# Kernel optimization log

Hardware: AMD Instinct MI355X
Metric: run time of the kernel (lower is better)

## Reference

```python
import jax, jax.numpy as jnp
import numpy as np


def setup_inputs() -> dict:
    key = jax.random.key(0)
    k1, k2, k3, k4 = jax.random.split(key, 4)
    in_f, out_f, rank, tokens = 4096, 4096, 256, 8192
    bound = 1.0 / np.sqrt(in_f)
    x = jax.random.normal(k1, (tokens, in_f), dtype=jnp.float32)
    U = jax.random.uniform(k2, (out_f, rank), dtype=jnp.float32, minval=-bound, maxval=bound)
    V = jax.random.uniform(k3, (rank, in_f), dtype=jnp.float32, minval=-bound, maxval=bound)
    bias = jax.random.uniform(k4, (out_f,), dtype=jnp.float32, minval=-bound, maxval=bound)
    return {"x": x, "U": U, "V": V, "bias": bias}


def reference(x, U, V, bias):
    # Faithful to original: materialize W = U @ V, then F.linear(x, W, bias) = x @ W.T + bias
    W = U @ V                      # [out, in]
    return x @ W.T + bias          # [tokens, out]
```

## Files before the change

kernel.cpp:

```cpp
#include <hip/hip_runtime.h>
#include <stdint.h>

#define TOKENS 8192
#define INF    4096
#define OUTF   4096
#define RANK   256

typedef __attribute__((ext_vector_type(8))) short bf16x8;
typedef __attribute__((ext_vector_type(4))) float f32x4;

__device__ __forceinline__ unsigned short f2bf(float f) {
    union { float f; unsigned int u; } v; v.f = f;
    unsigned int r = v.u + 0x7FFFu + ((v.u >> 16) & 1u);
    return (unsigned short)(r >> 16);
}

__device__ __forceinline__ void gl_lds16(const void* g, void* l) {
    __builtin_amdgcn_global_load_lds(
        (const __attribute__((address_space(1))) unsigned int*)g,
        (__attribute__((address_space(3))) unsigned int*)l, 16, 0, 0);
}

__global__ void cvt4(const float4* __restrict__ va, ushort4* __restrict__ oa, int na,
                     const float4* __restrict__ vb, ushort4* __restrict__ ob) {
    int i = blockIdx.x * blockDim.x + threadIdx.x;
    float4 v;
    if (i < na) v = va[i]; else v = vb[i - na];
    ushort4 o;
    o.x = f2bf(v.x); o.y = f2bf(v.y); o.z = f2bf(v.z); o.w = f2bf(v.w);
    if (i < na) oa[i] = o; else ob[i - na] = o;
}

#define G1_BM 32
#define G1_BK 128
#define A1_STR 136

__device__ __forceinline__ void g1_stageV(const unsigned short* __restrict__ Vb,
                                          unsigned short* vdst, int kk,
                                          int wid, int lane) {
    #pragma unroll
    for (int j = 0; j < 8; ++j) {
        int r0  = wid * 32 + j * 4;
        int row = r0 + (lane >> 4);
        int c   = (lane & 15) ^ (row & 7);
        gl_lds16(Vb + (size_t)row * INF + kk + c * 8, vdst + r0 * G1_BK);
    }
}

__device__ __forceinline__ void g1_pack(float4 a, float4 b, unsigned short* dst) {
    union { bf16x8 v; unsigned short s[8]; } pk;
    pk.s[0] = f2bf(a.x); pk.s[1] = f2bf(a.y);
    pk.s[2] = f2bf(a.z); pk.s[3] = f2bf(a.w);
    pk.s[4] = f2bf(b.x); pk.s[5] = f2bf(b.y);
    pk.s[6] = f2bf(b.z); pk.s[7] = f2bf(b.w);
    *(bf16x8*)dst = pk.v;
}

__device__ __forceinline__ void g1_compute(f32x4 (&acc)[2][2],
                                           const unsigned short* vbuf,
                                           const unsigned short* abuf,
                                           int l15, int quad, int wid) {
    const int rr0 = wid * 32 + l15;
    const int sw  = l15 & 7;
    #pragma unroll
    for (int ks = 0; ks < 4; ++ks) {
        int p = ((ks * 4 + quad) ^ sw) * 8;
        bf16x8 v0 = *(const bf16x8*)&vbuf[rr0 * G1_BK + p];
        bf16x8 v1 = *(const bf16x8*)&vbuf[(rr0 + 16) * G1_BK + p];
        bf16x8 b0 = *(const bf16x8*)&abuf[l15 * A1_STR + ks * 32 + quad * 8];
        bf16x8 b1 = *(const bf16x8*)&abuf[(16 + l15) * A1_STR + ks * 32 + quad * 8];
        acc[0][0] = __builtin_amdgcn_mfma_f32_16x16x32_bf16(v0, b0, acc[0][0], 0, 0, 0);
        acc[0][1] = __builtin_amdgcn_mfma_f32_16x16x32_bf16(v0, b1, acc[0][1], 0, 0, 0);
        acc[1][0] = __builtin_amdgcn_mfma_f32_16x16x32_bf16(v1, b0, acc[1][0], 0, 0, 0);
        acc[1][1] = __builtin_amdgcn_mfma_f32_16x16x32_bf16(v1, b1, acc[1][1], 0, 0, 0);
    }
}

__global__ __launch_bounds__(512) void gemm1(const float* __restrict__ x,
                                             const unsigned short* __restrict__ Vb,
                                             unsigned short* __restrict__ T) {
    __shared__ __align__(16) unsigned short V0[RANK * G1_BK];
    __shared__ __align__(16) unsigned short V1[RANK * G1_BK];
    __shared__ __align__(16) unsigned short A0[G1_BM * A1_STR];
    __shared__ __align__(16) unsigned short A1[G1_BM * A1_STR];

    const int tid  = threadIdx.x;
    const int lane = tid & 63;
    const int wid  = tid >> 6;
    const int m0   = blockIdx.x * G1_BM;
    const int l15  = lane & 15;
    const int quad = lane >> 4;

    const int arow = tid >> 4;
    const int aseg = tid & 15;
    const float* xp = x + (size_t)(m0 + arow) * INF + aseg * 8;
    unsigned short* aw0 = &A0[arow * A1_STR + aseg * 8];
    unsigned short* aw1 = &A1[arow * A1_STR + aseg * 8];

    f32x4 acc[2][2];
    #pragma unroll
    for (int i = 0; i < 2; ++i)
        #pragma unroll
        for (int j = 0; j < 2; ++j) acc[i][j] = (f32x4){0.f, 0.f, 0.f, 0.f};

    g1_stageV(Vb, V0, 0, wid, lane);
    float4 xr0 = *(const float4*)(xp);
    float4 xr1 = *(const float4*)(xp + 4);
    g1_pack(xr0, xr1, aw0);

    for (int t = 0; t < 30; t += 2) {
        __syncthreads();
        g1_stageV(Vb, V1, (t + 1) * G1_BK, wid, lane);
        xr0 = *(const float4*)(xp + (t + 1) * G1_BK);
        xr1 = *(const float4*)(xp + (t + 1) * G1_BK + 4);
        g1_compute(acc, V0, A0, l15, quad, wid);
        g1_pack(xr0, xr1, aw1);

        __syncthreads();
        g1_stageV(Vb, V0, (t + 2) * G1_BK, wid, lane);
        xr0 = *(const float4*)(xp + (t + 2) * G1_BK);
        xr1 = *(const float4*)(xp + (t + 2) * G1_BK + 4);
        g1_compute(acc, V1, A1, l15, quad, wid);
        g1_pack(xr0, xr1, aw0);
    }
    __syncthreads();
    g1_stageV(Vb, V1, 31 * G1_BK, wid, lane);
    xr0 = *(const float4*)(xp + 31 * G1_BK);
    xr1 = *(const float4*)(xp + 31 * G1_BK + 4);
    g1_compute(acc, V0, A0, l15, quad, wid);
    g1_pack(xr0, xr1, aw1);
    __syncthreads();
    g1_compute(acc, V1, A1, l15, quad, wid);

    #pragma unroll
    for (int mv = 0; mv < 2; ++mv) {
        #pragma unroll
        for (int mx = 0; mx < 2; ++mx) {
            int m = m0 + mx * 16 + l15;
            int n = wid * 32 + mv * 16 + quad * 4;
            ushort4 o;
            o.x = f2bf(acc[mv][mx][0]); o.y = f2bf(acc[mv][mx][1]);
            o.z = f2bf(acc[mv][mx][2]); o.w = f2bf(acc[mv][mx][3]);
            *(ushort4*)&T[(size_t)m * RANK + n] = o;
        }
    }
}

#define G2_BM 128
#define G2_BN 128
#define G2_BK 64

__device__ __forceinline__ void g2_stage(unsigned short (&Tl)[2][G2_BM * G2_BK],
                                         unsigned short (&Ul)[2][G2_BN * G2_BK],
                                         int b, int kk,
                                         const unsigned short* Tb,
                                         const unsigned short* Ub,
                                         int m0, int n0, int wid, int lrow, int cf) {
    #pragma unroll
    for (int j = 0; j < 4; ++j) {
        int r0 = wid * 32 + j * 8;
        gl_lds16(Tb + (size_t)(m0 + r0 + lrow) * RANK + kk + cf * 8, &Tl[b][r0 * G2_BK]);
        gl_lds16(Ub + (size_t)(n0 + r0 + lrow) * RANK + kk + cf * 8, &Ul[b][r0 * G2_BK]);
    }
}

__global__ __launch_bounds__(256) void gemm2(const unsigned short* __restrict__ Tb,
                                             const unsigned short* __restrict__ Ub,
                                             const float* __restrict__ bias,
                                             float* __restrict__ out) {
    __shared__ __align__(16) unsigned short Tlds[2][G2_BM * G2_BK];
    __shared__ __align__(16) unsigned short Ulds[2][G2_BN * G2_BK];

    const int tid  = threadIdx.x;
    const int lane = tid & 63;
    const int wid  = tid >> 6;
    const int wy   = wid >> 1, wx = wid & 1;
    const int m0   = blockIdx.y * G2_BM;
    const int n0   = blockIdx.x * G2_BN;
    const int l15  = lane & 15, quad = lane >> 4;
    const int lrow = lane >> 3;
    const int cf   = (lane & 7) ^ lrow;

    f32x4 acc[4][4];
    #pragma unroll
    for (int i = 0; i < 4; i++)
        #pragma unroll
        for (int j = 0; j < 4; j++) acc[i][j] = (f32x4){0.f, 0.f, 0.f, 0.f};

    float4 bv[4];
    #pragma unroll
    for (int nt = 0; nt < 4; ++nt)
        bv[nt] = *(const float4*)&bias[n0 + wx * 64 + nt * 16 + quad * 4];

    g2_stage(Tlds, Ulds, 0, 0, Tb, Ub, m0, n0, wid, lrow, cf);

    #pragma unroll
    for (int t = 0; t < 4; ++t) {
        __syncthreads();
        if (t < 3)
            g2_stage(Tlds, Ulds, (t + 1) & 1, (t + 1) * G2_BK,
                     Tb, Ub, m0, n0, wid, lrow, cf);
        const int b = t & 1;
        #pragma unroll
        for (int ks = 0; ks < 2; ++ks) {
            bf16x8 aU[4], bT[4];
            #pragma unroll
            for (int tt = 0; tt < 4; ++tt) {
                int ur = wx * 64 + tt * 16 + l15;
                int up = (ks * 4 + quad) ^ (ur & 7);
                aU[tt] = *(const bf16x8*)&Ulds[b][ur * G2_BK + up * 8];
                int tr = wy * 64 + tt * 16 + l15;
                int tp = (ks * 4 + quad) ^ (tr & 7);
                bT[tt] = *(const bf16x8*)&Tlds[b][tr * G2_BK + tp * 8];
            }
            #pragma unroll
            for (int nt = 0; nt < 4; ++nt)
                #pragma unroll
                for (int mt = 0; mt < 4; ++mt)
                    acc[nt][mt] = __builtin_amdgcn_mfma_f32_16x16x32_bf16(
                        aU[nt], bT[mt], acc[nt][mt], 0, 0, 0);
        }
    }

    #pragma unroll
    for (int nt = 0; nt < 4; ++nt) {
        int n_base = n0 + wx * 64 + nt * 16 + quad * 4;
        #pragma unroll
        for (int mt = 0; mt < 4; ++mt) {
            int m = m0 + wy * 64 + mt * 16 + l15;
            float4 v;
            v.x = acc[nt][mt][0] + bv[nt].x;
            v.y = acc[nt][mt][1] + bv[nt].y;
            v.z = acc[nt][mt][2] + bv[nt].z;
            v.w = acc[nt][mt][3] + bv[nt].w;
            *(float4*)&out[(size_t)m * OUTF + n_base] = v;
        }
    }
}

extern "C" void kernel_launch(void* const* d_in, const int* in_sizes, int n_in,
                              void* d_out, int out_size, void* d_ws, size_t ws_size,
                              hipStream_t stream) {
    const float* x    = (const float*)d_in[0];
    const float* U    = (const float*)d_in[1];
    const float* V    = (const float*)d_in[2];
    const float* bias = (const float*)d_in[3];
    float* out = (float*)d_out;

    unsigned short* Vb = (unsigned short*)d_ws;
    unsigned short* Ub = Vb + (size_t)RANK * INF;
    unsigned short* Tb = Ub + (size_t)OUTF * RANK;

    const int nv = RANK * INF / 4;
    const int nu = OUTF * RANK / 4;
    cvt4<<<(nv + nu) / 256, 256, 0, stream>>>((const float4*)V, (ushort4*)Vb, nv,
                                              (const float4*)U, (ushort4*)Ub);
    gemm1<<<TOKENS / G1_BM, 512, 0, stream>>>(x, Vb, Tb);
    gemm2<<<dim3(OUTF / G2_BN, TOKENS / G2_BM), 256, 0, stream>>>(Tb, Ub, bias, out);
}
```

Baseline: 284.2 us.

## Fuse both low-rank GEMMs into one kernel keeping T tile in LDS

Merges gemm1 (x@V^T) and gemm2 (T@U^T + bias) into one kernel. Each 32-token block computes its rank-256 T tile, stores it swizzled in shared memory, holds it in registers, then streams all of U through double-buffered LDS to write the full output rows. This drops the global round trip for T and one launch, and x prefetch moves one stage earlier. In exchange each block now reads all of U, only 256 blocks run with launch_bounds(512,2), and the second phase uses small per-wave tiles that may reuse U poorly.

Result: slower. 332.4 us (+17.0%).

```diff
diff --git a/kernel.cpp b/kernel.cpp
--- a/kernel.cpp
+++ b/kernel.cpp
@@ -31,19 +31,40 @@
     if (i < na) oa[i] = o; else ob[i - na] = o;
 }
 
-#define G1_BM 32
-#define G1_BK 128
-#define A1_STR 136
-
-__device__ __forceinline__ void g1_stageV(const unsigned short* __restrict__ Vb,
-                                          unsigned short* vdst, int kk,
-                                          int wid, int lane) {
+#define BM   32
+#define BK   128
+#define ASTR 136
+
+#define VB0 0
+#define VB1 32768
+#define AB0 65536
+#define AB1 (65536 + 4352)
+#define TB0 65536
+#define SMSZ 74240
+
+__device__ __forceinline__ void stageV(const unsigned short* __restrict__ Vb,
+                                       unsigned short* vdst, int kk,
+                                       int wid, int lane) {
     #pragma unroll
     for (int j = 0; j < 8; ++j) {
         int r0  = wid * 32 + j * 4;
         int row = r0 + (lane >> 4);
         int c   = (lane & 15) ^ (row & 7);
-        gl_lds16(Vb + (size_t)row * INF + kk + c * 8, vdst + r0 * G1_BK);
+        gl_lds16(Vb + (size_t)row * INF + kk + c * 8, vdst + r0 * BK);
+    }
+}
+
+__device__ __forceinline__ void stageU(const unsigned short* __restrict__ Ub,
+                                       unsigned short* udst, int nb,
+                                       int wid, int lane) {
+    int rp = lane >> 5;
+    int c  = lane & 31;
+    #pragma unroll
+    for (int j = 0; j < 8; ++j) {
+        int r0  = wid * 16 + j * 2;
+        int row = r0 + rp;
+        int sc  = c ^ (row & 7);
+        gl_lds16(Ub + (size_t)(nb + row) * RANK + sc * 8, udst + r0 * RANK);
     }
 }
 
@@ -65,10 +86,10 @@
     #pragma unroll
     for (int ks = 0; ks < 4; ++ks) {
         int p = ((ks * 4 + quad) ^ sw) * 8;
-        bf16x8 v0 = *(const bf16x8*)&vbuf[rr0 * G1_BK + p];
-        bf16x8 v1 = *(const bf16x8*)&vbuf[(rr0 + 16) * G1_BK + p];
-        bf16x8 b0 = *(const bf16x8*)&abuf[l15 * A1_STR + ks * 32 + quad * 8];
-        bf16x8 b1 = *(const bf16x8*)&abuf[(16 + l15) * A1_STR + ks * 32 + quad * 8];
+        bf16x8 v0 = *(const bf16x8*)&vbuf[rr0 * BK + p];
+        bf16x8 v1 = *(const bf16x8*)&vbuf[(rr0 + 16) * BK + p];
+        bf16x8 b0 = *(const bf16x8*)&abuf[l15 * ASTR + ks * 32 + quad * 8];
+        bf16x8 b1 = *(const bf16x8*)&abuf[(16 + l15) * ASTR + ks * 32 + quad * 8];
         acc[0][0] = __builtin_amdgcn_mfma_f32_16x16x32_bf16(v0, b0, acc[0][0], 0, 0, 0);
         acc[0][1] = __builtin_amdgcn_mfma_f32_16x16x32_bf16(v0, b1, acc[0][1], 0, 0, 0);
         acc[1][0] = __builtin_amdgcn_mfma_f32_16x16x32_bf16(v1, b0, acc[1][0], 0, 0, 0);
@@ -76,26 +97,49 @@
     }
 }
 
-__global__ __launch_bounds__(512) void gemm1(const float* __restrict__ x,
-                                             const unsigned short* __restrict__ Vb,
-                                             unsigned short* __restrict__ T) {
-    __shared__ __align__(16) unsigned short V0[RANK * G1_BK];
-    __shared__ __align__(16) unsigned short V1[RANK * G1_BK];
-    __shared__ __align__(16) unsigned short A0[G1_BM * A1_STR];
-    __shared__ __align__(16) unsigned short A1[G1_BM * A1_STR];
+__device__ __forceinline__ void p2_body(const bf16x8 (&tf)[8][2],
+                                        const unsigned short* ubuf,
+                                        float* __restrict__ out,
+                                        const float* __restrict__ bias,
+                                        int m0, int nb, int wid, int l15, int quad) {
+    f32x4 a0 = (f32x4){0.f, 0.f, 0.f, 0.f};
+    f32x4 a1 = (f32x4){0.f, 0.f, 0.f, 0.f};
+    const int ub = (wid * 16 + l15) * RANK;
+    const int sw = l15 & 7;
+    #pragma unroll
+    for (int ks = 0; ks < 8; ++ks) {
+        bf16x8 uf = *(const bf16x8*)&ubuf[ub + (((ks * 4 + quad) ^ sw) * 8)];
+        a0 = __builtin_amdgcn_mfma_f32_16x16x32_bf16(uf, tf[ks][0], a0, 0, 0, 0);
+        a1 = __builtin_amdgcn_mfma_f32_16x16x32_bf16(uf, tf[ks][1], a1, 0, 0, 0);
+    }
+    const int nc = nb + wid * 16 + quad * 4;
+    float4 bb = *(const float4*)&bias[nc];
+    float4 v0, v1;
+    v0.x = a0[0] + bb.x; v0.y = a0[1] + bb.y; v0.z = a0[2] + bb.z; v0.w = a0[3] + bb.w;
+    v1.x = a1[0] + bb.x; v1.y = a1[1] + bb.y; v1.z = a1[2] + bb.z; v1.w = a1[3] + bb.w;
+    *(float4*)&out[(size_t)(m0 + l15) * OUTF + nc] = v0;
+    *(float4*)&out[(size_t)(m0 + 16 + l15) * OUTF + nc] = v1;
+}
+
+__global__ __launch_bounds__(512, 2) void fused(const float* __restrict__ x,
+                                                const unsigned short* __restrict__ Vb,
+                                                const unsigned short* __restrict__ Ub,
+                                                const float* __restrict__ bias,
+                                                float* __restrict__ out) {
+    __shared__ __align__(16) unsigned short SM[SMSZ];
 
     const int tid  = threadIdx.x;
     const int lane = tid & 63;
     const int wid  = tid >> 6;
-    const int m0   = blockIdx.x * G1_BM;
+    const int m0   = blockIdx.x * BM;
     const int l15  = lane & 15;
     const int quad = lane >> 4;
 
     const int arow = tid >> 4;
     const int aseg = tid & 15;
     const float* xp = x + (size_t)(m0 + arow) * INF + aseg * 8;
-    unsigned short* aw0 = &A0[arow * A1_STR + aseg * 8];
-    unsigned short* aw1 = &A1[arow * A1_STR + aseg * 8];
+    unsigned short* aw0 = &SM[AB0 + arow * ASTR + aseg * 8];
+    unsigned short* aw1 = &SM[AB1 + arow * ASTR + aseg * 8];
 
     f32x4 acc[2][2];
     #pragma unroll
@@ -103,138 +147,71 @@
         #pragma unroll
         for (int j = 0; j < 2; ++j) acc[i][j] = (f32x4){0.f, 0.f, 0.f, 0.f};
 
-    g1_stageV(Vb, V0, 0, wid, lane);
-    float4 xr0 = *(const float4*)(xp);
-    float4 xr1 = *(const float4*)(xp + 4);
-    g1_pack(xr0, xr1, aw0);
-
+    stageV(Vb, SM + VB0, 0, wid, lane);
+    float4 pA0 = *(const float4*)(xp);
+    float4 pA1 = *(const float4*)(xp + 4);
+    g1_pack(pA0, pA1, aw0);
+    pA0 = *(const float4*)(xp + BK);
+    pA1 = *(const float4*)(xp + BK + 4);
+    float4 pB0, pB1;
+
+    #pragma unroll 1
     for (int t = 0; t < 30; t += 2) {
         __syncthreads();
-        g1_stageV(Vb, V1, (t + 1) * G1_BK, wid, lane);
-        xr0 = *(const float4*)(xp + (t + 1) * G1_BK);
-        xr1 = *(const float4*)(xp + (t + 1) * G1_BK + 4);
-        g1_compute(acc, V0, A0, l15, quad, wid);
-        g1_pack(xr0, xr1, aw1);
+        pB0 = *(const float4*)(xp + (t + 2) * BK);
+        pB1 = *(const float4*)(xp + (t + 2) * BK + 4);
+        stageV(Vb, SM + VB1, (t + 1) * BK, wid, lane);
+        g1_compute(acc, SM + VB0, SM + AB0, l15, quad, wid);
+        g1_pack(pA0, pA1, aw1);
 
         __syncthreads();
-        g1_stageV(Vb, V0, (t + 2) * G1_BK, wid, lane);
-        xr0 = *(const float4*)(xp + (t + 2) * G1_BK);
-        xr1 = *(const float4*)(xp + (t + 2) * G1_BK + 4);
-        g1_compute(acc, V1, A1, l15, quad, wid);
-        g1_pack(xr0, xr1, aw0);
-    }
-    __syncthreads();
-    g1_stageV(Vb, V1, 31 * G1_BK, wid, lane);
-    xr0 = *(const float4*)(xp + 31 * G1_BK);
-    xr1 = *(const float4*)(xp + 31 * G1_BK + 4);
-    g1_compute(acc, V0, A0, l15, quad, wid);
-    g1_pack(xr0, xr1, aw1);
-    __syncthreads();
-    g1_compute(acc, V1, A1, l15, quad, wid);
-
-    #pragma unroll
-    for (int mv = 0; mv < 2; ++mv) {
+        pA0 = *(const float4*)(xp + (t + 3) * BK);
+        pA1 = *(const float4*)(xp + (t + 3) * BK + 4);
+        stageV(Vb, SM + VB0, (t + 2) * BK, wid, lane);
+        g1_compute(acc, SM + VB1, SM + AB1, l15, quad, wid);
+        g1_pack(pB0, pB1, aw0);
+    }
+    __syncthreads();
+    stageV(Vb, SM + VB1, 31 * BK, wid, lane);
+    g1_compute(acc, SM + VB0, SM + AB0, l15, quad, wid);
+    g1_pack(pA0, pA1, aw1);
+    __syncthreads();
+    stageU(Ub, SM + VB0, 0, wid, lane);
+    g1_compute(acc, SM + VB1, SM + AB1, l15, quad, wid);
+    __syncthreads();
+
+    #pragma unroll
+    for (int mv = 0; mv < 2; ++mv)
         #pragma unroll
         for (int mx = 0; mx < 2; ++mx) {
-            int m = m0 + mx * 16 + l15;
-            int n = wid * 32 + mv * 16 + quad * 4;
+            int tok = mx * 16 + l15;
+            int cc  = wid * 4 + mv * 2 + (quad >> 1);
+            int sc  = cc ^ (tok & 7);
             ushort4 o;
             o.x = f2bf(acc[mv][mx][0]); o.y = f2bf(acc[mv][mx][1]);
             o.z = f2bf(acc[mv][mx][2]); o.w = f2bf(acc[mv][mx][3]);
-            *(ushort4*)&T[(size_t)m * RANK + n] = o;
+            *(ushort4*)&SM[TB0 + tok * RANK + sc * 8 + (quad & 1) * 4] = o;
         }
-    }
-}
-
-#define G2_BM 128
-#define G2_BN 128
-#define G2_BK 64
-
-__device__ __forceinline__ void g2_stage(unsigned short (&Tl)[2][G2_BM * G2_BK],
-                                         unsigned short (&Ul)[2][G2_BN * G2_BK],
-                                         int b, int kk,
-                                         const unsigned short* Tb,
-                                         const unsigned short* Ub,
-                                         int m0, int n0, int wid, int lrow, int cf) {
-    #pragma unroll
-    for (int j = 0; j < 4; ++j) {
-        int r0 = wid * 32 + j * 8;
-        gl_lds16(Tb + (size_t)(m0 + r0 + lrow) * RANK + kk + cf * 8, &Tl[b][r0 * G2_BK]);
-        gl_lds16(Ub + (size_t)(n0 + r0 + lrow) * RANK + kk + cf * 8, &Ul[b][r0 * G2_BK]);
-    }
-}
-
-__global__ __launch_bounds__(256) void gemm2(const unsigned short* __restrict__ Tb,
-                                             const unsigned short* __restrict__ Ub,
-                                             const float* __restrict__ bias,
-                                             float* __restrict__ out) {
-    __shared__ __align__(16) unsigned short Tlds[2][G2_BM * G2_BK];
-    __shared__ __align__(16) unsigned short Ulds[2][G2_BN * G2_BK];
-
-    const int tid  = threadIdx.x;
-    const int lane = tid & 63;
-    const int wid  = tid >> 6;
-    const int wy   = wid >> 1, wx = wid & 1;
-    const int m0   = blockIdx.y * G2_BM;
-    const int n0   = blockIdx.x * G2_BN;
-    const int l15  = lane & 15, quad = lane >> 4;
-    const int lrow = lane >> 3;
-    const int cf   = (lane & 7) ^ lrow;
-
-    f32x4 acc[4][4];
-    #pragma unroll
-    for (int i = 0; i < 4; i++)
+    __syncthreads();
+
+    bf16x8 tf[8][2];
+    #pragma unroll
+    for (int ks = 0; ks < 8; ++ks)
         #pragma unroll
-        for (int j = 0; j < 4; j++) acc[i][j] = (f32x4){0.f, 0.f, 0.f, 0.f};
-
-    float4 bv[4];
-    #pragma unroll
-    for (int nt = 0; nt < 4; ++nt)
-        bv[nt] = *(const float4*)&bias[n0 + wx * 64 + nt * 16 + quad * 4];
-
-    g2_stage(Tlds, Ulds, 0, 0, Tb, Ub, m0, n0, wid, lrow, cf);
-
-    #pragma unroll
-    for (int t = 0; t < 4; ++t) {
+        for (int mt = 0; mt < 2; ++mt) {
+            int tok = mt * 16 + l15;
+            tf[ks][mt] = *(const bf16x8*)
+                &SM[TB0 + tok * RANK + (((ks * 4 + quad) ^ (l15 & 7)) * 8)];
+        }
+
+    #pragma unroll 1
+    for (int u = 0; u < 32; u += 2) {
+        if (u) __syncthreads();
+        stageU(Ub, SM + VB1, (u + 1) * 128, wid, lane);
+        p2_body(tf, SM + VB0, out, bias, m0, u * 128, wid, l15, quad);
         __syncthreads();
-        if (t < 3)
-            g2_stage(Tlds, Ulds, (t + 1) & 1, (t + 1) * G2_BK,
-                     Tb, Ub, m0, n0, wid, lrow, cf);
-        const int b = t & 1;
-        #pragma unroll
-        for (int ks = 0; ks < 2; ++ks) {
-            bf16x8 aU[4], bT[4];
-            #pragma unroll
-            for (int tt = 0; tt < 4; ++tt) {
-                int ur = wx * 64 + tt * 16 + l15;
-                int up = (ks * 4 + quad) ^ (ur & 7);
-                aU[tt] = *(const bf16x8*)&Ulds[b][ur * G2_BK + up * 8];
-                int tr = wy * 64 + tt * 16 + l15;
-                int tp = (ks * 4 + quad) ^ (tr & 7);
-                bT[tt] = *(const bf16x8*)&Tlds[b][tr * G2_BK + tp * 8];
-            }
-            #pragma unroll
-            for (int nt = 0; nt < 4; ++nt)
-                #pragma unroll
-                for (int mt = 0; mt < 4; ++mt)
-                    acc[nt][mt] = __builtin_amdgcn_mfma_f32_16x16x32_bf16(
-                        aU[nt], bT[mt], acc[nt][mt], 0, 0, 0);
-        }
-    }
-
-    #pragma unroll
-    for (int nt = 0; nt < 4; ++nt) {
-        int n_base = n0 + wx * 64 + nt * 16 + quad * 4;
-        #pragma unroll
-        for (int mt = 0; mt < 4; ++mt) {
-            int m = m0 + wy * 64 + mt * 16 + l15;
-            float4 v;
-            v.x = acc[nt][mt][0] + bv[nt].x;
-            v.y = acc[nt][mt][1] + bv[nt].y;
-            v.z = acc[nt][mt][2] + bv[nt].z;
-            v.w = acc[nt][mt][3] + bv[nt].w;
-            *(float4*)&out[(size_t)m * OUTF + n_base] = v;
-        }
+        if (u + 2 < 32) stageU(Ub, SM + VB0, (u + 2) * 128, wid, lane);
+        p2_body(tf, SM + VB1, out, bias, m0, (u + 1) * 128, wid, l15, quad);
     }
 }
 
@@ -249,12 +226,10 @@
 
     unsigned short* Vb = (unsigned short*)d_ws;
     unsigned short* Ub = Vb + (size_t)RANK * INF;
-    unsigned short* Tb = Ub + (size_t)OUTF * RANK;
 
     const int nv = RANK * INF / 4;
     const int nu = OUTF * RANK / 4;
     cvt4<<<(nv + nu) / 256, 256, 0, stream>>>((const float4*)V, (ushort4*)Vb, nv,
                                               (const float4*)U, (ushort4*)Ub);
-    gemm1<<<TOKENS / G1_BM, 512, 0, stream>>>(x, Vb, Tb);
-    gemm2<<<dim3(OUTF / G2_BN, TOKENS / G2_BM), 256, 0, stream>>>(Tb, Ub, bias, out);
-}
+    fused<<<TOKENS / BM, 512, 0, stream>>>(x, Vb, Ub, bias, out);
+}
```
